# Performance work log

Measured on AMD Instinct MI355X. Metric: run time of the kernel, lower is better.

## Reference

```python
import jax, jax.numpy as jnp
import numpy as np

DIM = 256
HEADS = 8
WIN = 8
N = WIN * WIN          # 64 tokens per window
NW = 1024              # windows per image (256x256 map, 8x8 windows)
BATCH = 4
B_ = BATCH * NW        # 4096
HEAD_DIM = DIM // HEADS


def _relative_position_index():
    # identical to the torch buffer construction in WindowAttention.__init__
    coords = np.stack(np.meshgrid(np.arange(WIN), np.arange(WIN), indexing='ij'))  # [2,W,W]
    flat = coords.reshape(2, -1)                                # [2, N]
    rel = flat[:, :, None] - flat[:, None, :]                   # [2, N, N]
    rel = rel.transpose(1, 2, 0).copy()                         # [N, N, 2]
    rel[:, :, 0] += WIN - 1
    rel[:, :, 1] += WIN - 1
    rel[:, :, 0] *= 2 * WIN - 1
    return jnp.asarray(rel.sum(-1), dtype=jnp.int32)            # [N, N], values in [0, 225)


def setup_inputs() -> dict:
    key = jax.random.key(0)
    ks = jax.random.split(key, 9)
    std = 0.02
    return {
        'x': jax.random.normal(ks[0], (B_, N, DIM), dtype=jnp.float32),
        'mask': jax.random.normal(ks[1], (NW, N, N), dtype=jnp.float32),
        'w_q': jax.random.normal(ks[2], (DIM, DIM), dtype=jnp.float32) * std,
        'b_q': jnp.zeros((DIM,), dtype=jnp.float32),
        'w_kv': jax.random.normal(ks[3], (2 * DIM, DIM), dtype=jnp.float32) * std,
        'b_kv': jnp.zeros((2 * DIM,), dtype=jnp.float32),
        'bias_table': jax.random.normal(ks[4], ((2 * WIN - 1) ** 2, HEADS), dtype=jnp.float32) * std,
        'w_o': jax.random.normal(ks[5], (DIM, DIM), dtype=jnp.float32) * std,
        'b_o': jnp.zeros((DIM,), dtype=jnp.float32),
        'rp_index': _relative_position_index(),
    }


def reference(x, mask, w_q, b_q, w_kv, b_kv, bias_table, w_o, b_o, rp_index):
    Bw, n, c = x.shape
    h, d = HEADS, c // HEADS
    scale = d ** -0.5

    # linear QKV projection (LinearProjection with attn_kv=None)
    q = (x @ w_q.T + b_q).reshape(Bw, n, h, d).transpose(0, 2, 1, 3)      # [B_, H, N, D]
    kv = (x @ w_kv.T + b_kv).reshape(Bw, n, 2, h, d).transpose(2, 0, 3, 1, 4)
    k, v = kv[0], kv[1]                                                    # [B_, H, N, D]

    # scaled QK^T
    attn = jnp.einsum('bhnd,bhmd->bhnm', q * scale, k)                     # [B_, H, N, N]

    # gathered relative position bias (ratio = 1 since attn_kv is None)
    bias = bias_table[rp_index]                                            # [N, N, H]
    attn = attn + bias.transpose(2, 0, 1)[None]                            # broadcast over B_

    # per-window additive mask
    nW = mask.shape[0]
    attn = attn.reshape(Bw // nW, nW, h, n, n) + mask[None, :, None]
    attn = attn.reshape(Bw, h, n, n)

    attn = jax.nn.softmax(attn, axis=-1)

    out = jnp.einsum('bhnm,bhmd->bhnd', attn, v)                           # [B_, H, N, D]
    out = out.transpose(0, 2, 1, 3).reshape(Bw, n, c)
    return out @ w_o.T + b_o
```

## Files before the change

### kernel.cpp

```cpp
#include <hip/hip_runtime.h>
#include <hip/hip_bf16.h>
#include <stdint.h>

typedef __bf16 bf16_t;
typedef bf16_t bf16x8 __attribute__((ext_vector_type(8)));
typedef bf16_t bf16x4 __attribute__((ext_vector_type(4)));
typedef bf16_t bf16x2 __attribute__((ext_vector_type(2)));
typedef float f32x4 __attribute__((ext_vector_type(4)));
typedef uint32_t u32x4 __attribute__((ext_vector_type(4)));

#define WS_WKV_OFF 65536
#define WS_WO_OFF  196608
#define WS_B8_OFF  524288
#define QSCALE 0.17677669529663687f

__global__ __launch_bounds__(256) void prep_kernel(
    const float* __restrict__ wq, const float* __restrict__ wkv,
    const float* __restrict__ wo, const float* __restrict__ bt,
    const int* __restrict__ rp,
    bf16_t* __restrict__ wsq, bf16_t* __restrict__ wskv,
    bf16_t* __restrict__ wso, float* __restrict__ bias8) {
  int t = blockIdx.x * 256 + threadIdx.x;
  if (t < 65536)  wsq[t]  = (bf16_t)(wq[t] * QSCALE);
  if (t < 131072) wskv[t] = (bf16_t)wkv[t];
  if (t < 65536)  wso[t]  = (bf16_t)wo[t];
  if (t < 4096) {
    int idx = rp[t];
#pragma unroll
    for (int h = 0; h < 8; ++h) bias8[h * 4096 + t] = bt[idx * 8 + h];
  }
}

__device__ __forceinline__ bf16x8 xpose_frag(uint32_t e0, uint32_t e1,
                                             uint32_t o0, uint32_t o1,
                                             int ad0, int ad1, bool hi) {
  uint32_t v0e = (uint32_t)__builtin_amdgcn_ds_bpermute(ad0, (int)e0);
  uint32_t v0o = (uint32_t)__builtin_amdgcn_ds_bpermute(ad0, (int)o0);
  uint32_t v1e = (uint32_t)__builtin_amdgcn_ds_bpermute(ad0, (int)e1);
  uint32_t v1o = (uint32_t)__builtin_amdgcn_ds_bpermute(ad0, (int)o1);
  uint32_t v2e = (uint32_t)__builtin_amdgcn_ds_bpermute(ad1, (int)e0);
  uint32_t v2o = (uint32_t)__builtin_amdgcn_ds_bpermute(ad1, (int)o0);
  uint32_t v3e = (uint32_t)__builtin_amdgcn_ds_bpermute(ad1, (int)e1);
  uint32_t v3o = (uint32_t)__builtin_amdgcn_ds_bpermute(ad1, (int)o1);
  u32x4 r;
  r.x = hi ? v0o : v0e;
  r.y = hi ? v1o : v1e;
  r.z = hi ? v2o : v2e;
  r.w = hi ? v3o : v3e;
  return __builtin_bit_cast(bf16x8, r);
}

__device__ __forceinline__ uint32_t pk2(float a, float b) {
  bf16x2 t = {(bf16_t)a, (bf16_t)b};
  return __builtin_bit_cast(uint32_t, t);
}

__global__ __launch_bounds__(512, 2) void win_attn_kernel(
    const float* __restrict__ x, const float* __restrict__ mask,
    const float* __restrict__ bq, const float* __restrict__ bkv,
    const float* __restrict__ bo,
    const bf16_t* __restrict__ wsq, const bf16_t* __restrict__ wskv,
    const bf16_t* __restrict__ wso, const float* __restrict__ bias8,
    float* __restrict__ out) {
  __shared__ bf16_t lds[35328];
  const int b    = blockIdx.x;
  const int tid  = threadIdx.x;
  const int h    = tid >> 6;
  const int lane = tid & 63;
  const int lrow = lane & 15;
  const int lgrp = lane >> 4;
  const bool hi  = (lgrp & 2) != 0;
  const int ad0  = ((((2 * lgrp) & 3) << 4) + lrow) << 2;
  const int ad1  = ((((2 * lgrp + 1) & 3) << 4) + lrow) << 2;
  const f32x4 zf = {0.f, 0.f, 0.f, 0.f};

  {
    const float4* xv = (const float4*)(x + (size_t)b * 16384);
#pragma unroll
    for (int j = 0; j < 8; ++j) {
      int i4 = j * 512 + tid;
      float4 v = xv[i4];
      int e = i4 * 4;
      int r = e >> 8, c = e & 255;
      bf16x4 w = {(bf16_t)v.x, (bf16_t)v.y, (bf16_t)v.z, (bf16_t)v.w};
      *(bf16x4*)(lds + r * 264 + c) = w;
    }
  }
  __syncthreads();

  bf16_t* ldsVt = lds + 16896 + h * 2304;

  {
    const bf16_t* WVh = wskv + (256 + h * 32) * 256;
    float bv0 = bkv[256 + h * 32 + lrow];
    float bv1 = bkv[256 + h * 32 + 16 + lrow];
#pragma unroll
    for (int vh = 0; vh < 2; ++vh) {
      f32x4 av[2][2];
      av[0][0] = av[0][1] = av[1][0] = av[1][1] = zf;
#pragma unroll
      for (int ks = 0; ks < 8; ++ks) {
        bf16x8 xa[2];
#pragma unroll
        for (int i = 0; i < 2; ++i)
          xa[i] = *(const bf16x8*)(lds + ((vh * 2 + i) * 16 + lrow) * 264 + ks * 32 + lgrp * 8);
        bf16x8 wvf[2];
#pragma unroll
        for (int tn = 0; tn < 2; ++tn)
          wvf[tn] = *(const bf16x8*)(WVh + (tn * 16 + lrow) * 256 + ks * 32 + lgrp * 8);
#pragma unroll
        for (int i = 0; i < 2; ++i)
#pragma unroll
          for (int tn = 0; tn < 2; ++tn)
            av[i][tn] = __builtin_amdgcn_mfma_f32_16x16x32_bf16(xa[i], wvf[tn], av[i][tn], 0, 0, 0);
      }
#pragma unroll
      for (int i = 0; i < 2; ++i)
#pragma unroll
        for (int tn = 0; tn < 2; ++tn) {
          float bv = tn ? bv1 : bv0;
          bf16x4 vv;
#pragma unroll
          for (int r = 0; r < 4; ++r) vv[r] = (bf16_t)(av[i][tn][r] + bv);
          *(bf16x4*)(ldsVt + (tn * 16 + lrow) * 72 + (vh * 2 + i) * 16 + lgrp * 4) = vv;
        }
    }
  }

  bf16x8 qb[4], ka[4];
  {
    const bf16_t* WQh = wsq  + h * 32 * 256;
    const bf16_t* WKh = wskv + h * 32 * 256;
#pragma unroll
    for (int nt = 0; nt < 4; ++nt) {
      f32x4 aq[2], ak2[2];
      aq[0] = aq[1] = ak2[0] = ak2[1] = zf;
#pragma unroll
      for (int ks = 0; ks < 8; ++ks) {
        bf16x8 xb = *(const bf16x8*)(lds + (nt * 16 + lrow) * 264 + ks * 32 + lgrp * 8);
        bf16x8 wqf[2], wkf[2];
#pragma unroll
        for (int tm = 0; tm < 2; ++tm) {
          int off = (tm * 16 + lrow) * 256 + ks * 32 + lgrp * 8;
          wqf[tm] = *(const bf16x8*)(WQh + off);
          wkf[tm] = *(const bf16x8*)(WKh + off);
        }
#pragma unroll
        for (int tm = 0; tm < 2; ++tm) {
          aq[tm]  = __builtin_amdgcn_mfma_f32_16x16x32_bf16(wqf[tm], xb, aq[tm], 0, 0, 0);
          ak2[tm] = __builtin_amdgcn_mfma_f32_16x16x32_bf16(wkf[tm], xb, ak2[tm], 0, 0, 0);
        }
      }
      uint32_t pq[2][2], pk[2][2];
#pragma unroll
      for (int tm = 0; tm < 2; ++tm) {
        float4 b4 = *(const float4*)(bq + h * 32 + tm * 16 + lgrp * 4);
        float4 k4 = *(const float4*)(bkv + h * 32 + tm * 16 + lgrp * 4);
        pq[tm][0] = pk2(aq[tm][0] + b4.x * QSCALE, aq[tm][1] + b4.y * QSCALE);
        pq[tm][1] = pk2(aq[tm][2] + b4.z * QSCALE, aq[tm][3] + b4.w * QSCALE);
        pk[tm][0] = pk2(ak2[tm][0] + k4.x, ak2[tm][1] + k4.y);
        pk[tm][1] = pk2(ak2[tm][2] + k4.z, ak2[tm][3] + k4.w);
      }
      qb[nt] = xpose_frag(pq[0][0], pq[0][1], pq[1][0], pq[1][1], ad0, ad1, hi);
      ka[nt] = xpose_frag(pk[0][0], pk[0][1], pk[1][0], pk[1][1], ad0, ad1, hi);
    }
  }

  __syncthreads();

  const float* maskw = mask + (size_t)(b & 1023) * 4096;
  const float* biash = bias8 + h * 4096;
#pragma unroll
  for (int qt = 0; qt < 4; ++qt) {
    f32x4 st[4];
#pragma unroll
    for (int tm = 0; tm < 4; ++tm)
      st[tm] = __builtin_amdgcn_mfma_f32_16x16x32_bf16(ka[tm], qb[qt], zf, 0, 0, 0);
    int q = qt * 16 + lrow;
    float sm = 0.f;
#pragma unroll
    for (int tm = 0; tm < 4; ++tm) {
      int kb = tm * 16 + lgrp * 4;
      float4 mb = *(const float4*)(maskw + q * 64 + kb);
      float4 bb = *(const float4*)(biash + q * 64 + kb);
#pragma unroll
      for (int r = 0; r < 4; ++r) {
        float madd = (r == 0) ? (mb.x + bb.x) : (r == 1) ? (mb.y + bb.y)
                   : (r == 2) ? (mb.z + bb.z) : (mb.w + bb.w);
        float p = __expf(st[tm][r] + madd);
        st[tm][r] = p;
        sm += p;
      }
    }
    sm += __shfl_xor(sm, 16);
    sm += __shfl_xor(sm, 32);
    float rs = 1.0f / sm;
    uint32_t ppk[4][2];
#pragma unroll
    for (int tm = 0; tm < 4; ++tm) {
      ppk[tm][0] = pk2(st[tm][0] * rs, st[tm][1] * rs);
      ppk[tm][1] = pk2(st[tm][2] * rs, st[tm][3] * rs);
    }
    bf16x8 paf[2];
#pragma unroll
    for (int kf = 0; kf < 2; ++kf)
      paf[kf] = xpose_frag(ppk[2 * kf][0], ppk[2 * kf][1],
                           ppk[2 * kf + 1][0], ppk[2 * kf + 1][1], ad0, ad1, hi);
    f32x4 o[2] = {zf, zf};
#pragma unroll
    for (int dt = 0; dt < 2; ++dt)
#pragma unroll
      for (int kf = 0; kf < 2; ++kf) {
        bf16x8 vf = *(const bf16x8*)(ldsVt + (dt * 16 + lrow) * 72 + kf * 32 + lgrp * 8);
        o[dt] = __builtin_amdgcn_mfma_f32_16x16x32_bf16(paf[kf], vf, o[dt], 0, 0, 0);
      }
#pragma unroll
    for (int dt = 0; dt < 2; ++dt)
#pragma unroll
      for (int r = 0; r < 4; ++r)
        lds[(qt * 16 + lgrp * 4 + r) * 264 + h * 32 + dt * 16 + lrow] = (bf16_t)o[dt][r];
  }
  __syncthreads();

  const int nb = h * 32;
  float* outw = out + (size_t)b * 16384;
#pragma unroll
  for (int half = 0; half < 2; ++half) {
    f32x4 oc[2][2];
#pragma unroll
    for (int tm = 0; tm < 2; ++tm)
#pragma unroll
      for (int tn = 0; tn < 2; ++tn) oc[tm][tn] = zf;
#pragma unroll
    for (int ks = 0; ks < 8; ++ks) {
      bf16x8 ao[2];
#pragma unroll
      for (int tm = 0; tm < 2; ++tm)
        ao[tm] = *(const bf16x8*)(lds + ((half * 2 + tm) * 16 + lrow) * 264 + ks * 32 + lgrp * 8);
      bf16x8 bw[2];
#pragma unroll
      for (int tn = 0; tn < 2; ++tn)
        bw[tn] = *(const bf16x8*)(wso + (nb + tn * 16 + lrow) * 256 + ks * 32 + lgrp * 8);
#pragma unroll
      for (int tm = 0; tm < 2; ++tm)
#pragma unroll
        for (int tn = 0; tn < 2; ++tn)
          oc[tm][tn] = __builtin_amdgcn_mfma_f32_16x16x32_bf16(ao[tm], bw[tn], oc[tm][tn], 0, 0, 0);
    }
#pragma unroll
    for (int tn = 0; tn < 2; ++tn) {
      float bov = bo[nb + tn * 16 + lrow];
#pragma unroll
      for (int tm = 0; tm < 2; ++tm)
#pragma unroll
        for (int r = 0; r < 4; ++r)
          outw[((half * 2 + tm) * 16 + lgrp * 4 + r) * 256 + nb + tn * 16 + lrow] =
              oc[tm][tn][r] + bov;
    }
  }
}

extern "C" void kernel_launch(void* const* d_in, const int* in_sizes, int n_in,
                              void* d_out, int out_size, void* d_ws, size_t ws_size,
                              hipStream_t stream) {
  const float* x    = (const float*)d_in[0];
  const float* mask = (const float*)d_in[1];
  const float* wq   = (const float*)d_in[2];
  const float* bq   = (const float*)d_in[3];
  const float* wkv  = (const float*)d_in[4];
  const float* bkv  = (const float*)d_in[5];
  const float* bt   = (const float*)d_in[6];
  const float* wo   = (const float*)d_in[7];
  const float* bo   = (const float*)d_in[8];
  const int*   rp   = (const int*)d_in[9];
  float* out = (float*)d_out;

  bf16_t* wsq  = (bf16_t*)d_ws;
  bf16_t* wskv = wsq + WS_WKV_OFF;
  bf16_t* wso  = wsq + WS_WO_OFF;
  float*  bias8 = (float*)((char*)d_ws + WS_B8_OFF);

  prep_kernel<<<512, 256, 0, stream>>>(wq, wkv, wo, bt, rp, wsq, wskv, wso, bias8);

  win_attn_kernel<<<4096, 512, 0, stream>>>(
      x, mask, bq, bkv, bo, wsq, wskv, wso, bias8, out);
}
```

Before: 561.8 us.

## Split Q/K projection loops and raise occupancy hint to four blocks per CU

Raises the launch-bounds minimum blocks per CU from 2 to 4, pushing the compiler to cap registers near 64 VGPRs per thread. It also restructures the Q and K projection: instead of computing both Q and K per 16-row tile, it runs separate Q and K passes, each handling two row tiles per weight fragment load, which halves global weight-fragment reads and reuses each weight fragment across two MFMAs. LDS use (about 69 KB per block) may still limit residency to fewer than four blocks, and the tighter register cap risks spills.

```diff
diff --git a/kernel.cpp b/kernel.cpp
--- a/kernel.cpp
+++ b/kernel.cpp
@@ -55,7 +55,7 @@
   return __builtin_bit_cast(uint32_t, t);
 }
 
-__global__ __launch_bounds__(512, 2) void win_attn_kernel(
+__global__ __launch_bounds__(512, 4) void win_attn_kernel(
     const float* __restrict__ x, const float* __restrict__ mask,
     const float* __restrict__ bq, const float* __restrict__ bkv,
     const float* __restrict__ bo,
@@ -129,40 +129,77 @@
 
   bf16x8 qb[4], ka[4];
   {
-    const bf16_t* WQh = wsq  + h * 32 * 256;
-    const bf16_t* WKh = wskv + h * 32 * 256;
-#pragma unroll
-    for (int nt = 0; nt < 4; ++nt) {
-      f32x4 aq[2], ak2[2];
-      aq[0] = aq[1] = ak2[0] = ak2[1] = zf;
+    const bf16_t* WQh = wsq + h * 32 * 256;
+#pragma unroll
+    for (int qh = 0; qh < 2; ++qh) {
+      f32x4 aq[2][2];
+      aq[0][0] = aq[0][1] = aq[1][0] = aq[1][1] = zf;
 #pragma unroll
       for (int ks = 0; ks < 8; ++ks) {
-        bf16x8 xb = *(const bf16x8*)(lds + (nt * 16 + lrow) * 264 + ks * 32 + lgrp * 8);
-        bf16x8 wqf[2], wkf[2];
-#pragma unroll
-        for (int tm = 0; tm < 2; ++tm) {
-          int off = (tm * 16 + lrow) * 256 + ks * 32 + lgrp * 8;
-          wqf[tm] = *(const bf16x8*)(WQh + off);
-          wkf[tm] = *(const bf16x8*)(WKh + off);
-        }
-#pragma unroll
-        for (int tm = 0; tm < 2; ++tm) {
-          aq[tm]  = __builtin_amdgcn_mfma_f32_16x16x32_bf16(wqf[tm], xb, aq[tm], 0, 0, 0);
-          ak2[tm] = __builtin_amdgcn_mfma_f32_16x16x32_bf16(wkf[tm], xb, ak2[tm], 0, 0, 0);
-        }
-      }
-      uint32_t pq[2][2], pk[2][2];
+        bf16x8 xb[2];
+#pragma unroll
+        for (int i = 0; i < 2; ++i)
+          xb[i] = *(const bf16x8*)(lds + ((qh * 2 + i) * 16 + lrow) * 264 + ks * 32 + lgrp * 8);
+        bf16x8 wqf[2];
+#pragma unroll
+        for (int tm = 0; tm < 2; ++tm)
+          wqf[tm] = *(const bf16x8*)(WQh + (tm * 16 + lrow) * 256 + ks * 32 + lgrp * 8);
+#pragma unroll
+        for (int tm = 0; tm < 2; ++tm)
+#pragma unroll
+          for (int i = 0; i < 2; ++i)
+            aq[tm][i] = __builtin_amdgcn_mfma_f32_16x16x32_bf16(wqf[tm], xb[i], aq[tm][i], 0, 0, 0);
+      }
+      uint32_t pq[2][2][2];
 #pragma unroll
       for (int tm = 0; tm < 2; ++tm) {
         float4 b4 = *(const float4*)(bq + h * 32 + tm * 16 + lgrp * 4);
+#pragma unroll
+        for (int i = 0; i < 2; ++i) {
+          pq[tm][i][0] = pk2(aq[tm][i][0] + b4.x * QSCALE, aq[tm][i][1] + b4.y * QSCALE);
+          pq[tm][i][1] = pk2(aq[tm][i][2] + b4.z * QSCALE, aq[tm][i][3] + b4.w * QSCALE);
+        }
+      }
+#pragma unroll
+      for (int i = 0; i < 2; ++i)
+        qb[qh * 2 + i] = xpose_frag(pq[0][i][0], pq[0][i][1], pq[1][i][0], pq[1][i][1], ad0, ad1, hi);
+    }
+  }
+  {
+    const bf16_t* WKh = wskv + h * 32 * 256;
+#pragma unroll
+    for (int kh = 0; kh < 2; ++kh) {
+      f32x4 ak2[2][2];
+      ak2[0][0] = ak2[0][1] = ak2[1][0] = ak2[1][1] = zf;
+#pragma unroll
+      for (int ks = 0; ks < 8; ++ks) {
+        bf16x8 xb[2];
+#pragma unroll
+        for (int i = 0; i < 2; ++i)
+          xb[i] = *(const bf16x8*)(lds + ((kh * 2 + i) * 16 + lrow) * 264 + ks * 32 + lgrp * 8);
+        bf16x8 wkf[2];
+#pragma unroll
+        for (int tm = 0; tm < 2; ++tm)
+          wkf[tm] = *(const bf16x8*)(WKh + (tm * 16 + lrow) * 256 + ks * 32 + lgrp * 8);
+#pragma unroll
+        for (int tm = 0; tm < 2; ++tm)
+#pragma unroll
+          for (int i = 0; i < 2; ++i)
+            ak2[tm][i] = __builtin_amdgcn_mfma_f32_16x16x32_bf16(wkf[tm], xb[i], ak2[tm][i], 0, 0, 0);
+      }
+      uint32_t pk[2][2][2];
+#pragma unroll
+      for (int tm = 0; tm < 2; ++tm) {
         float4 k4 = *(const float4*)(bkv + h * 32 + tm * 16 + lgrp * 4);
-        pq[tm][0] = pk2(aq[tm][0] + b4.x * QSCALE, aq[tm][1] + b4.y * QSCALE);
-        pq[tm][1] = pk2(aq[tm][2] + b4.z * QSCALE, aq[tm][3] + b4.w * QSCALE);
-        pk[tm][0] = pk2(ak2[tm][0] + k4.x, ak2[tm][1] + k4.y);
-        pk[tm][1] = pk2(ak2[tm][2] + k4.z, ak2[tm][3] + k4.w);
-      }
-      qb[nt] = xpose_frag(pq[0][0], pq[0][1], pq[1][0], pq[1][1], ad0, ad1, hi);
-      ka[nt] = xpose_frag(pk[0][0], pk[0][1], pk[1][0], pk[1][1], ad0, ad1, hi);
+#pragma unroll
+        for (int i = 0; i < 2; ++i) {
+          pk[tm][i][0] = pk2(ak2[tm][i][0] + k4.x, ak2[tm][i][1] + k4.y);
+          pk[tm][i][1] = pk2(ak2[tm][i][2] + k4.z, ak2[tm][i][3] + k4.w);
+        }
+      }
+#pragma unroll
+      for (int i = 0; i < 2; ++i)
+        ka[kh * 2 + i] = xpose_frag(pk[0][i][0], pk[0][i][1], pk[1][i][0], pk[1][i][1], ad0, ad1, hi);
     }
   }
 
```

Measured after the change: 568.5 us. Within noise of the previous version (+1.2%).
